# Kernel optimization log

Hardware: AMD Instinct MI355X
Metric: run time of the kernel (lower is better)

## Reference

```python
import jax, jax.numpy as jnp
import numpy as np

L, B, E = 128, 16, 512
C_OUT = 64
KERNELS = [1, 3, 5, 7]
M = len(KERNELS) * C_OUT          # mlpdec_in = 256
OUT_SIZE = 256
SLOPE = 0.1


def setup_inputs() -> dict:
    key = jax.random.key(0)
    ks = jax.random.split(key, 32)
    s = 0.02
    d = {"x": jax.random.normal(ks[0], (L, B, E), dtype=jnp.float32)}
    # conv branches: weight (C_out, 1, k, E), bias (C_out,)
    for i, k in enumerate(KERNELS):
        d[f"cw{i}"] = jax.random.normal(ks[1 + 2 * i], (C_OUT, 1, k, E), dtype=jnp.float32) * s
        d[f"cb{i}"] = jnp.zeros((C_OUT,), dtype=jnp.float32)
    dims = [(C_OUT, 2 * M), (C_OUT, C_OUT), (C_OUT, C_OUT), (C_OUT, C_OUT)]
    for i, (o, inn) in enumerate(dims):
        d[f"mw{i}"] = jax.random.normal(ks[10 + 2 * i], (o, inn), dtype=jnp.float32) * s
        d[f"mb{i}"] = jnp.zeros((o,), dtype=jnp.float32)
    # mlp_layer: Linear(C->C), Linear(C->output_size)
    d["lw0"] = jax.random.normal(ks[20], (C_OUT, C_OUT), dtype=jnp.float32) * s
    d["lb0"] = jnp.zeros((C_OUT,), dtype=jnp.float32)
    d["lw1"] = jax.random.normal(ks[21], (OUT_SIZE, C_OUT), dtype=jnp.float32) * s
    d["lb1"] = jnp.zeros((OUT_SIZE,), dtype=jnp.float32)
    return d


def _lrelu(x):
    return jax.nn.leaky_relu(x, SLOPE)


def _conv_branch(xb, w, b):
    # xb: (B,1,L,E), w: (C,1,k,E) -> (B,C,L)
    k = w.shape[2]
    pad = (k - 1) // 2
    y = jax.lax.conv_general_dilated(
        xb, w, window_strides=(1, 1), padding=[(pad, pad), (0, 0)],
        dimension_numbers=("NCHW", "OIHW", "NCHW"))
    return _lrelu(y[..., 0] + b[None, :, None])


def reference(x, cw0, cb0, cw1, cb1, cw2, cb2, cw3, cb3,
              mw0, mb0, mw1, mb1, mw2, mb2, mw3, mb3,
              lw0, lb0, lw1, lb1):
    # x: (L,B,E) -> (B,1,L,E)
    xb = jnp.transpose(x, (1, 0, 2))[:, None, :, :]
    feats = jnp.concatenate([
        _conv_branch(xb, cw0, cb0), _conv_branch(xb, cw1, cb1),
        _conv_branch(xb, cw2, cb2), _conv_branch(xb, cw3, cb3)], axis=1)  # (B, 4C, L)
    f = jnp.transpose(feats, (2, 0, 1))  # (L, B, M)
    # pairwise: pair[i, j] = [f[j], f[i]]  -> (L, L, B, 2M)
    a = jnp.broadcast_to(f[None, :, :, :], (L, L, B, M))
    bpart = jnp.broadcast_to(f[:, None, :, :], (L, L, B, M))
    h = jnp.concatenate([a, bpart], axis=-1)
    for w, bb in ((mw0, mb0), (mw1, mb1), (mw2, mb2), (mw3, mb3)):
        h = _lrelu(h @ w.T + bb)
    h = h.sum(axis=0)  # (L, B, C)
    h = _lrelu(h @ lw0.T + lb0)
    return _lrelu(h @ lw1.T + lb1)  # (L, B, OUT_SIZE)
```

## Files before the change

### kernel.cpp

```cpp
#include <hip/hip_runtime.h>
#include <hip/hip_bf16.h>

#define SLOPE 0.1f
typedef unsigned short u16;
typedef unsigned int u32;
typedef __attribute__((ext_vector_type(8))) short short8;
typedef __attribute__((ext_vector_type(4))) float floatx4;

__device__ __forceinline__ float lrelu(float x) { return x > 0.0f ? x : SLOPE * x; }

__device__ __forceinline__ void split_rn(float x, u16* h, u16* l) {
    union { __hip_bfloat16 b; u16 u; } c1, c2;
    c1.b = __float2bfloat16(x);
    float hf = __bfloat162float(c1.b);
    c2.b = __float2bfloat16(x - hf);
    *h = c1.u; *l = c2.u;
}

__device__ __forceinline__ void pack2x2(float v0, float v1, u32& h, u32& l) {
    u32 a0 = __float_as_uint(v0), a1 = __float_as_uint(v1);
    h = __builtin_amdgcn_perm(a1, a0, 0x07060302u);
    float r0 = v0 - __uint_as_float(a0 & 0xFFFF0000u);
    float r1 = v1 - __uint_as_float(a1 & 0xFFFF0000u);
    l = __builtin_amdgcn_perm(__float_as_uint(r1), __float_as_uint(r0), 0x07060302u);
}

__device__ __forceinline__ short8 load_frag(const u16* p) {
    union { uint4 q; short8 s; } cv;
    cv.q = *(const uint4*)p;
    return cv.s;
}

__device__ __forceinline__ floatx4 mfma16(short8 a, short8 b, floatx4 c) {
    return __builtin_amdgcn_mfma_f32_16x16x32_bf16(a, b, c, 0, 0, 0);
}

__global__ __launch_bounds__(256) void p0_prep(
    const float* __restrict__ x,
    const float* __restrict__ cw0, const float* __restrict__ cw1,
    const float* __restrict__ cw2, const float* __restrict__ cw3,
    const float* __restrict__ mw0, const float* __restrict__ mw1,
    const float* __restrict__ mw2, const float* __restrict__ mw3,
    const float* __restrict__ lw0, const float* __restrict__ lw1,
    u16* __restrict__ xfh, u16* __restrict__ xfl,
    u16* __restrict__ wcfh, u16* __restrict__ wcfl,
    u16* __restrict__ b2fh, u16* __restrict__ b2fl,
    u16* __restrict__ w3fh, u16* __restrict__ w3fl,
    float* __restrict__ lw0t, float* __restrict__ lw1t)
{
    int idx = (blockIdx.x * 256 + threadIdx.x) * 4;
    if (idx < 1048576) {
        const int j = idx & 7, lane = (idx >> 3) & 63;
        const int kc = (idx >> 9) & 15, rt = idx >> 13;
        const int l15 = lane & 15, quad = lane >> 4;
        const float4 s = *(const float4*)(x + (rt * 16 + l15) * 512 + kc * 32 + quad * 8 + j);
        u16 h[4], l[4];
        split_rn(s.x, &h[0], &l[0]); split_rn(s.y, &h[1], &l[1]);
        split_rn(s.z, &h[2], &l[2]); split_rn(s.w, &h[3], &l[3]);
        *(ushort4*)(xfh + idx) = make_ushort4(h[0], h[1], h[2], h[3]);
        *(ushort4*)(xfl + idx) = make_ushort4(l[0], l[1], l[2], l[3]);
        return;
    }
    idx -= 1048576;
    if (idx < 524288) {
        const int j = idx & 7, lane = (idx >> 3) & 63;
        const int kc = (idx >> 9) & 15, nt = (idx >> 13) & 3, slot = idx >> 15;
        int branch, base;
        if (slot == 0)      { branch = 0; base = 0; }
        else if (slot < 4)  { branch = 1; base = 1; }
        else if (slot < 9)  { branch = 2; base = 4; }
        else                { branch = 3; base = 9; }
        const int dk = slot - base, ksz = 2 * branch + 1;
        const float* cw = branch == 0 ? cw0 : branch == 1 ? cw1 : branch == 2 ? cw2 : cw3;
        const int c = nt * 16 + (lane & 15);
        const int e = kc * 32 + (lane >> 4) * 8 + j;
        const float4 s = *(const float4*)(cw + (c * ksz + dk) * 512 + e);
        u16 h[4], l[4];
        split_rn(s.x, &h[0], &l[0]); split_rn(s.y, &h[1], &l[1]);
        split_rn(s.z, &h[2], &l[2]); split_rn(s.w, &h[3], &l[3]);
        *(ushort4*)(wcfh + idx) = make_ushort4(h[0], h[1], h[2], h[3]);
        *(ushort4*)(wcfl + idx) = make_ushort4(l[0], l[1], l[2], l[3]);
        return;
    }
    idx -= 524288;
    if (idx < 32768) {
        const int j = idx & 7, lane = (idx >> 3) & 63;
        const int kc = (idx >> 9) & 7, nt = (idx >> 12) & 3, nh = idx >> 14;
        const int n = nh * 64 + nt * 16 + (lane & 15);
        const int k = kc * 32 + (lane >> 4) * 8 + j;
        const float4 s = *(const float4*)(mw0 + (n & 63) * 512 + (n >> 6) * 256 + k);
        u16 h[4], l[4];
        split_rn(s.x, &h[0], &l[0]); split_rn(s.y, &h[1], &l[1]);
        split_rn(s.z, &h[2], &l[2]); split_rn(s.w, &h[3], &l[3]);
        *(ushort4*)(b2fh + idx) = make_ushort4(h[0], h[1], h[2], h[3]);
        *(ushort4*)(b2fl + idx) = make_ushort4(l[0], l[1], l[2], l[3]);
        return;
    }
    idx -= 32768;
    if (idx < 12288) {
        const int j = idx & 7, lane = (idx >> 3) & 63;
        const int kc = (idx >> 9) & 1, mt = (idx >> 10) & 3, layer = idx >> 12;
        const float* mw = layer == 0 ? mw1 : layer == 1 ? mw2 : mw3;
        const int ch = mt * 16 + (lane & 15);
        const int k = kc * 32 + (lane >> 4) * 8 + j;
        const float4 s = *(const float4*)(mw + ch * 64 + k);
        u16 h[4], l[4];
        split_rn(s.x, &h[0], &l[0]); split_rn(s.y, &h[1], &l[1]);
        split_rn(s.z, &h[2], &l[2]); split_rn(s.w, &h[3], &l[3]);
        *(ushort4*)(w3fh + idx) = make_ushort4(h[0], h[1], h[2], h[3]);
        *(ushort4*)(w3fl + idx) = make_ushort4(l[0], l[1], l[2], l[3]);
        return;
    }
    idx -= 12288;
    if (idx < 4096) {
        const int k = idx >> 6, n = idx & 63;
        float4 o;
        o.x = lw0[(n + 0) * 64 + k]; o.y = lw0[(n + 1) * 64 + k];
        o.z = lw0[(n + 2) * 64 + k]; o.w = lw0[(n + 3) * 64 + k];
        *(float4*)(lw0t + idx) = o;
        return;
    }
    idx -= 4096;
    if (idx < 16384) {
        const int k = idx >> 8, n = idx & 255;
        float4 o;
        o.x = lw1[(n + 0) * 64 + k]; o.y = lw1[(n + 1) * 64 + k];
        o.z = lw1[(n + 2) * 64 + k]; o.w = lw1[(n + 3) * 64 + k];
        *(float4*)(lw1t + idx) = o;
        return;
    }
}

__global__ __launch_bounds__(512) void k1f_conv(
    const u16* __restrict__ xfh, const u16* __restrict__ xfl,
    const u16* __restrict__ wcfh, const u16* __restrict__ wcfl,
    float* __restrict__ Fp)
{
    __shared__ float P[8][16][72];

    const int t = threadIdx.x, lane = t & 63, w = t >> 6;
    const int rtp = blockIdx.x;
    const int slot = blockIdx.y;
    int br, base;
    if (slot == 0)      { br = 0; base = 0; }
    else if (slot < 4)  { br = 1; base = 1; }
    else if (slot < 9)  { br = 2; base = 4; }
    else                { br = 3; base = 9; }
    const int dk = slot - base;
    const int l15 = lane & 15, quad = lane >> 4;

    floatx4 acc[2][4];
    #pragma unroll
    for (int r = 0; r < 2; ++r)
        #pragma unroll
        for (int j = 0; j < 4; ++j) acc[r][j] = (floatx4)0.0f;

    #pragma unroll
    for (int kk = 0; kk < 2; ++kk) {
        const int kc = w * 2 + kk;
        short8 bh[4], bl[4];
        #pragma unroll
        for (int nt = 0; nt < 4; ++nt) {
            const int boff = (((slot * 4 + nt) * 16 + kc) * 64 + lane) * 8;
            bh[nt] = load_frag(wcfh + boff);
            bl[nt] = load_frag(wcfl + boff);
        }
        #pragma unroll
        for (int r = 0; r < 2; ++r) {
            const int rts = rtp + r * 64 + dk - br;
            if (rts < 0 || rts >= 128) continue;
            const int aoff = ((rts * 16 + kc) * 64 + lane) * 8;
            const short8 ah = load_frag(xfh + aoff);
            const short8 al = load_frag(xfl + aoff);
            #pragma unroll
            for (int nt = 0; nt < 4; ++nt) {
                acc[r][nt] = mfma16(ah, bh[nt], acc[r][nt]);
                acc[r][nt] = mfma16(ah, bl[nt], acc[r][nt]);
                acc[r][nt] = mfma16(al, bh[nt], acc[r][nt]);
            }
        }
    }

    #pragma unroll
    for (int r = 0; r < 2; ++r) {
        #pragma unroll
        for (int nt = 0; nt < 4; ++nt)
            #pragma unroll
            for (int rr = 0; rr < 4; ++rr)
                P[w][quad * 4 + rr][nt * 16 + l15] = acc[r][nt][rr];
        __syncthreads();
        if (t < 256) {
            const int row = t >> 4, c4 = (t & 15) * 4;
            float4 o;
            #pragma unroll
            for (int i = 0; i < 4; ++i) {
                float val = P[0][row][c4 + i];
                #pragma unroll
                for (int ww = 1; ww < 8; ++ww) val += P[ww][row][c4 + i];
                (&o.x)[i] = val;
            }
            const int rowg = (rtp + r * 64) * 16 + row;
            *(float4*)(Fp + (slot * 2048 + rowg) * 64 + c4) = o;
        }
        __syncthreads();
    }
}

__global__ __launch_bounds__(256) void kB_uv(
    const float* __restrict__ Fp,
    const u16* __restrict__ b2fh, const u16* __restrict__ b2fl,
    const float* __restrict__ cb0, const float* __restrict__ cb1,
    const float* __restrict__ cb2, const float* __restrict__ cb3,
    const float* __restrict__ mb0,
    float* __restrict__ u, float* __restrict__ v_t)
{
    __shared__ float P[4][16][17];

    const int t = threadIdx.x, lane = t & 63, w = t >> 6;
    const int bid = blockIdx.x;
    const int rt = bid >> 3;
    const int nh = (bid >> 2) & 1;
    const int nt = bid & 3;
    const int l15 = lane & 15, quad = lane >> 4;

    floatx4 acc = (floatx4)0.0f;

    #pragma unroll
    for (int kk = 0; kk < 2; ++kk) {
        const int kc = w * 2 + kk;
        const int br2 = kc >> 1;
        const int base2 = br2 * br2, ksz2 = 2 * br2 + 1;
        const int cc0 = (kc & 1) * 32 + quad * 8;
        const int row = rt * 16 + l15;

        float s[8];
        #pragma unroll
        for (int j = 0; j < 8; ++j) s[j] = 0.0f;
        for (int d = 0; d < ksz2; ++d) {
            const float* pp = Fp + ((base2 + d) * 2048 + row) * 64 + cc0;
            const float4 q0 = *(const float4*)pp;
            const float4 q1 = *(const float4*)(pp + 4);
            s[0] += q0.x; s[1] += q0.y; s[2] += q0.z; s[3] += q0.w;
            s[4] += q1.x; s[5] += q1.y; s[6] += q1.z; s[7] += q1.w;
        }
        const float* cb = br2 == 0 ? cb0 : br2 == 1 ? cb1 : br2 == 2 ? cb2 : cb3;
        union { u16 us[8]; short8 v; } AH, AL;
        #pragma unroll
        for (int j = 0; j < 8; ++j) {
            const float val = lrelu(s[j] + cb[cc0 + j]);
            split_rn(val, &AH.us[j], &AL.us[j]);
        }
        const short8 ah = AH.v, al = AL.v;

        const int boff = (((nh * 4 + nt) * 8 + kc) * 64 + lane) * 8;
        const short8 bh = load_frag(b2fh + boff);
        const short8 bl = load_frag(b2fl + boff);
        acc = mfma16(ah, bh, acc);
        acc = mfma16(ah, bl, acc);
        acc = mfma16(al, bh, acc);
    }

    #pragma unroll
    for (int rr = 0; rr < 4; ++rr)
        P[w][quad * 4 + rr][l15] = acc[rr];
    __syncthreads();

    {
        const int row = t >> 4, c = t & 15;
        const float val = P[0][row][c] + P[1][row][c] + P[2][row][c] + P[3][row][c];
        const int rglob = rt * 16 + row;
        const int ch = nt * 16 + c;
        if (nh == 0) {
            u[rglob * 64 + ch] = val + mb0[ch];
        } else {
            const int i = rglob >> 4, b = rglob & 15;
            v_t[(b * 128 + i) * 64 + ch] = val;
        }
    }
}

__global__ __launch_bounds__(256, 4) void k3_pair(
    const float* __restrict__ u, const float* __restrict__ v_t,
    const u16* __restrict__ w3fh, const u16* __restrict__ w3fl,
    const float* __restrict__ mb1, const float* __restrict__ mb2,
    const float* __restrict__ mb3,
    const float* __restrict__ lw0t, const float* __restrict__ lb0,
    const float* __restrict__ lw1t, const float* __restrict__ lb1,
    float* __restrict__ out)
{
    __shared__ __align__(16) u16 Hh[128][72];
    __shared__ __align__(16) u16 Hl[128][72];
    __shared__ float Sp[4][64];
    __shared__ float Ss[64];
    __shared__ float T1[64];

    const int t = threadIdx.x, lane = t & 63, w = t >> 6;
    const int jb = blockIdx.x, b = jb & 15;
    const int l15 = lane & 15, quad = lane >> 4;
    const int i0 = w * 32;
    const int c4 = l15 * 4;

    const float4 uu = *(const float4*)(u + jb * 64 + c4);

    const float* vb = v_t + (b * 128 + i0) * 64;
    #pragma unroll
    for (int n = 0; n < 8; ++n) {
        const int idx = n * 64 + lane;
        const int il = idx >> 4;
        const float4 vv = *(const float4*)(vb + idx * 4);
        const float a0 = lrelu(vv.x + uu.x), a1 = lrelu(vv.y + uu.y);
        const float a2 = lrelu(vv.z + uu.z), a3 = lrelu(vv.w + uu.w);
        u32 h01, l01, h23, l23;
        pack2x2(a0, a1, h01, l01);
        pack2x2(a2, a3, h23, l23);
        *(uint2*)&Hh[i0 + il][c4] = make_uint2(h01, h23);
        *(uint2*)&Hl[i0 + il][c4] = make_uint2(l01, l23);
    }

    const float* mbp[3] = {mb1, mb2, mb3};
    for (int layer = 0; layer < 3; ++layer) {
        floatx4 acc[4][2];
        #pragma unroll
        for (int i = 0; i < 4; ++i)
            #pragma unroll
            for (int j = 0; j < 2; ++j) acc[i][j] = (floatx4)0.0f;

        #pragma unroll
        for (int kc = 0; kc < 2; ++kc) {
            short8 ah[4], al[4];
            #pragma unroll
            for (int mt = 0; mt < 4; ++mt) {
                const int aoff = (((layer * 4 + mt) * 2 + kc) * 64 + lane) * 8;
                ah[mt] = load_frag(w3fh + aoff);
                al[mt] = load_frag(w3fl + aoff);
            }
            const int k0 = kc * 32 + quad * 8;
            #pragma unroll
            for (int nt = 0; nt < 2; ++nt) {
                const short8 bh = load_frag(&Hh[i0 + nt * 16 + l15][k0]);
                const short8 bl = load_frag(&Hl[i0 + nt * 16 + l15][k0]);
                #pragma unroll
                for (int mt = 0; mt < 4; ++mt) {
                    acc[mt][nt] = mfma16(ah[mt], bh, acc[mt][nt]);
                    acc[mt][nt] = mfma16(ah[mt], bl, acc[mt][nt]);
                    acc[mt][nt] = mfma16(al[mt], bh, acc[mt][nt]);
                }
            }
        }

        if (layer < 2) {
            #pragma unroll
            for (int mt = 0; mt < 4; ++mt) {
                float bias[4];
                #pragma unroll
                for (int r = 0; r < 4; ++r) bias[r] = mbp[layer][mt * 16 + quad * 4 + r];
                #pragma unroll
                for (int nt = 0; nt < 2; ++nt) {
                    const int i = i0 + nt * 16 + l15;
                    const float v0 = lrelu(acc[mt][nt][0] + bias[0]);
                    const float v1 = lrelu(acc[mt][nt][1] + bias[1]);
                    const float v2 = lrelu(acc[mt][nt][2] + bias[2]);
                    const float v3 = lrelu(acc[mt][nt][3] + bias[3]);
                    u32 h01, l01, h23, l23;
                    pack2x2(v0, v1, h01, l01);
                    pack2x2(v2, v3, h23, l23);
                    *(uint2*)&Hh[i][mt * 16 + quad * 4] = make_uint2(h01, h23);
                    *(uint2*)&Hl[i][mt * 16 + quad * 4] = make_uint2(l01, l23);
                }
            }
        } else {
            #pragma unroll
            for (int mt = 0; mt < 4; ++mt) {
                float bias[4];
                #pragma unroll
                for (int r = 0; r < 4; ++r) bias[r] = mbp[2][mt * 16 + quad * 4 + r];
                float4 sv;
                #pragma unroll
                for (int r = 0; r < 4; ++r) {
                    float val = lrelu(acc[mt][0][r] + bias[r])
                              + lrelu(acc[mt][1][r] + bias[r]);
                    val += __shfl_xor(val, 1, 16);
                    val += __shfl_xor(val, 2, 16);
                    val += __shfl_xor(val, 4, 16);
                    val += __shfl_xor(val, 8, 16);
                    (&sv.x)[r] = val;
                }
                if (l15 == 0)
                    *(float4*)(&Sp[w][mt * 16 + quad * 4]) = sv;
            }
        }
    }

    __syncthreads();
    if (t < 64) Ss[t] = Sp[0][t] + Sp[1][t] + Sp[2][t] + Sp[3][t];
    __syncthreads();
    if (t < 64) {
        float a = lb0[t];
        #pragma unroll 8
        for (int k = 0; k < 64; ++k) a += Ss[k] * lw0t[k * 64 + t];
        T1[t] = lrelu(a);
    }
    __syncthreads();
    {
        float a = lb1[t];
        #pragma unroll 8
        for (int k = 0; k < 64; ++k) a += T1[k] * lw1t[k * 256 + t];
        out[jb * 256 + t] = lrelu(a);
    }
}

extern "C" void kernel_launch(void* const* d_in, const int* in_sizes, int n_in,
                              void* d_out, int out_size, void* d_ws, size_t ws_size,
                              hipStream_t stream)
{
    const float* x   = (const float*)d_in[0];
    const float* cw0 = (const float*)d_in[1];
    const float* cb0 = (const float*)d_in[2];
    const float* cw1 = (const float*)d_in[3];
    const float* cb1 = (const float*)d_in[4];
    const float* cw2 = (const float*)d_in[5];
    const float* cb2 = (const float*)d_in[6];
    const float* cw3 = (const float*)d_in[7];
    const float* cb3 = (const float*)d_in[8];
    const float* mw0 = (const float*)d_in[9];
    const float* mb0 = (const float*)d_in[10];
    const float* mw1 = (const float*)d_in[11];
    const float* mb1 = (const float*)d_in[12];
    const float* mw2 = (const float*)d_in[13];
    const float* mb2 = (const float*)d_in[14];
    const float* mw3 = (const float*)d_in[15];
    const float* mb3 = (const float*)d_in[16];
    const float* lw0 = (const float*)d_in[17];
    const float* lb0 = (const float*)d_in[18];
    const float* lw1 = (const float*)d_in[19];
    const float* lb1 = (const float*)d_in[20];
    float* out = (float*)d_out;

    char* base = (char*)d_ws;
    u16* xfh   = (u16*)(base + 0);
    u16* xfl   = (u16*)(base + 2097152);
    u16* wcfh  = (u16*)(base + 4194304);
    u16* wcfl  = (u16*)(base + 5242880);
    u16* b2fh  = (u16*)(base + 6291456);
    u16* b2fl  = (u16*)(base + 6356992);
    u16* w3fh  = (u16*)(base + 6422528);
    u16* w3fl  = (u16*)(base + 6447104);
    float* lw0t  = (float*)(base + 6471680);
    float* lw1t  = (float*)(base + 6488064);
    float* Fp  = (float*)(base + 6553600);
    float* u   = (float*)(base + 14942208);
    float* v_t = (float*)(base + 15466496);

    hipLaunchKernelGGL(p0_prep, dim3(1600), dim3(256), 0, stream,
                       x, cw0, cw1, cw2, cw3, mw0, mw1, mw2, mw3, lw0, lw1,
                       xfh, xfl, wcfh, wcfl, b2fh, b2fl, w3fh, w3fl, lw0t, lw1t);
    hipLaunchKernelGGL(k1f_conv, dim3(64, 16), dim3(512), 0, stream,
                       xfh, xfl, wcfh, wcfl, Fp);
    hipLaunchKernelGGL(kB_uv, dim3(1024), dim3(256), 0, stream,
                       Fp, b2fh, b2fl, cb0, cb1, cb2, cb3, mb0, u, v_t);
    hipLaunchKernelGGL(k3_pair, dim3(2048), dim3(256), 0, stream,
                       u, v_t, w3fh, w3fl, mb1, mb2, mb3, lw0t, lb0, lw1t, lb1, out);
}
```

Measured before the change: 153.9 us.

## Pair two output rows per block, split i range, and combine via atomics

Each k3 block now processes two (j,b) output rows over half of the i range. This reuses every loaded weight fragment for twice as many MFMAs and halves the per-block i span. The two blocks that share a pair atomically accumulate their partial sums into a global buffer, and the block that arrives last (found with a counter) runs the final MLP layers. The global buffer and counters are zeroed inside kB_uv, reusing workspace that held xfh and is no longer needed by then. In exchange this adds global atomics, a threadfence, and a last-block handoff, and the float summation order is no longer deterministic.

After: 189.1 us. 1.23x slower.

```diff
diff --git a/kernel.cpp b/kernel.cpp
--- a/kernel.cpp
+++ b/kernel.cpp
@@ -212,12 +212,20 @@
     const float* __restrict__ cb0, const float* __restrict__ cb1,
     const float* __restrict__ cb2, const float* __restrict__ cb3,
     const float* __restrict__ mb0,
-    float* __restrict__ u, float* __restrict__ v_t)
+    float* __restrict__ u, float* __restrict__ v_t,
+    float* __restrict__ Sg, int* __restrict__ cnt)
 {
     __shared__ float P[4][16][17];
 
     const int t = threadIdx.x, lane = t & 63, w = t >> 6;
     const int bid = blockIdx.x;
+
+    {
+        const int gid = bid * 256 + t;
+        if (gid < 131072) Sg[gid] = 0.0f;
+        else if (gid < 132096) cnt[gid - 131072] = 0;
+    }
+
     const int rt = bid >> 3;
     const int nh = (bid >> 2) & 1;
     const int nt = bid & 3;
@@ -279,72 +287,91 @@
     }
 }
 
-__global__ __launch_bounds__(256, 4) void k3_pair(
+__global__ __launch_bounds__(256, 4) void k3_dual(
     const float* __restrict__ u, const float* __restrict__ v_t,
     const u16* __restrict__ w3fh, const u16* __restrict__ w3fl,
     const float* __restrict__ mb1, const float* __restrict__ mb2,
     const float* __restrict__ mb3,
     const float* __restrict__ lw0t, const float* __restrict__ lb0,
     const float* __restrict__ lw1t, const float* __restrict__ lb1,
+    float* __restrict__ Sg, int* __restrict__ cnt,
     float* __restrict__ out)
 {
-    __shared__ __align__(16) u16 Hh[128][72];
-    __shared__ __align__(16) u16 Hl[128][72];
-    __shared__ float Sp[4][64];
-    __shared__ float Ss[64];
-    __shared__ float T1[64];
+    __shared__ __align__(16) char smem[38912];
+    u16 (*Hh0)[72] = (u16(*)[72])(smem);
+    u16 (*Hl0)[72] = (u16(*)[72])(smem + 9216);
+    u16 (*Hh1)[72] = (u16(*)[72])(smem + 18432);
+    u16 (*Hl1)[72] = (u16(*)[72])(smem + 27648);
+    float (*Sp0)[64] = (float(*)[64])(smem + 36864);
+    float (*Sp1)[64] = (float(*)[64])(smem + 37888);
+    float *Ss0 = (float*)(smem + 36864);
+    float *T10 = (float*)(smem + 36864 + 256);
+    float *Ss1 = (float*)(smem + 37888);
+    float *T11 = (float*)(smem + 37888 + 256);
+    int   *flagp = (int*)(smem + 36864 + 512);
 
     const int t = threadIdx.x, lane = t & 63, w = t >> 6;
-    const int jb = blockIdx.x, b = jb & 15;
+    const int bid = blockIdx.x;
+    const int p = bid >> 1, half = bid & 1;
+    const int jb0 = p, jb1 = p + 1024, b = p & 15;
     const int l15 = lane & 15, quad = lane >> 4;
-    const int i0 = w * 32;
+    const int i0l = w * 16;
+    const int il15 = i0l + l15;
     const int c4 = l15 * 4;
 
-    const float4 uu = *(const float4*)(u + jb * 64 + c4);
-
-    const float* vb = v_t + (b * 128 + i0) * 64;
+    const float4 uu0 = *(const float4*)(u + jb0 * 64 + c4);
+    const float4 uu1 = *(const float4*)(u + jb1 * 64 + c4);
+
+    const float* vb = v_t + (b * 128 + half * 64 + i0l) * 64;
     #pragma unroll
-    for (int n = 0; n < 8; ++n) {
+    for (int n = 0; n < 4; ++n) {
         const int idx = n * 64 + lane;
         const int il = idx >> 4;
         const float4 vv = *(const float4*)(vb + idx * 4);
-        const float a0 = lrelu(vv.x + uu.x), a1 = lrelu(vv.y + uu.y);
-        const float a2 = lrelu(vv.z + uu.z), a3 = lrelu(vv.w + uu.w);
-        u32 h01, l01, h23, l23;
-        pack2x2(a0, a1, h01, l01);
-        pack2x2(a2, a3, h23, l23);
-        *(uint2*)&Hh[i0 + il][c4] = make_uint2(h01, h23);
-        *(uint2*)&Hl[i0 + il][c4] = make_uint2(l01, l23);
+        {
+            const float a0 = lrelu(vv.x + uu0.x), a1 = lrelu(vv.y + uu0.y);
+            const float a2 = lrelu(vv.z + uu0.z), a3 = lrelu(vv.w + uu0.w);
+            u32 h01, l01, h23, l23;
+            pack2x2(a0, a1, h01, l01);
+            pack2x2(a2, a3, h23, l23);
+            *(uint2*)&Hh0[i0l + il][c4] = make_uint2(h01, h23);
+            *(uint2*)&Hl0[i0l + il][c4] = make_uint2(l01, l23);
+        }
+        {
+            const float a0 = lrelu(vv.x + uu1.x), a1 = lrelu(vv.y + uu1.y);
+            const float a2 = lrelu(vv.z + uu1.z), a3 = lrelu(vv.w + uu1.w);
+            u32 h01, l01, h23, l23;
+            pack2x2(a0, a1, h01, l01);
+            pack2x2(a2, a3, h23, l23);
+            *(uint2*)&Hh1[i0l + il][c4] = make_uint2(h01, h23);
+            *(uint2*)&Hl1[i0l + il][c4] = make_uint2(l01, l23);
+        }
     }
 
     const float* mbp[3] = {mb1, mb2, mb3};
     for (int layer = 0; layer < 3; ++layer) {
-        floatx4 acc[4][2];
-        #pragma unroll
-        for (int i = 0; i < 4; ++i)
-            #pragma unroll
-            for (int j = 0; j < 2; ++j) acc[i][j] = (floatx4)0.0f;
+        floatx4 acc0[4], acc1[4];
+        #pragma unroll
+        for (int i = 0; i < 4; ++i) { acc0[i] = (floatx4)0.0f; acc1[i] = (floatx4)0.0f; }
 
         #pragma unroll
         for (int kc = 0; kc < 2; ++kc) {
-            short8 ah[4], al[4];
+            const int k0 = kc * 32 + quad * 8;
+            const short8 bh0 = load_frag(&Hh0[il15][k0]);
+            const short8 bl0 = load_frag(&Hl0[il15][k0]);
+            const short8 bh1 = load_frag(&Hh1[il15][k0]);
+            const short8 bl1 = load_frag(&Hl1[il15][k0]);
             #pragma unroll
             for (int mt = 0; mt < 4; ++mt) {
                 const int aoff = (((layer * 4 + mt) * 2 + kc) * 64 + lane) * 8;
-                ah[mt] = load_frag(w3fh + aoff);
-                al[mt] = load_frag(w3fl + aoff);
-            }
-            const int k0 = kc * 32 + quad * 8;
-            #pragma unroll
-            for (int nt = 0; nt < 2; ++nt) {
-                const short8 bh = load_frag(&Hh[i0 + nt * 16 + l15][k0]);
-                const short8 bl = load_frag(&Hl[i0 + nt * 16 + l15][k0]);
-                #pragma unroll
-                for (int mt = 0; mt < 4; ++mt) {
-                    acc[mt][nt] = mfma16(ah[mt], bh, acc[mt][nt]);
-                    acc[mt][nt] = mfma16(ah[mt], bl, acc[mt][nt]);
-                    acc[mt][nt] = mfma16(al[mt], bh, acc[mt][nt]);
-                }
+                const short8 ah = load_frag(w3fh + aoff);
+                const short8 al = load_frag(w3fl + aoff);
+                acc0[mt] = mfma16(ah, bh0, acc0[mt]);
+                acc0[mt] = mfma16(ah, bl0, acc0[mt]);
+                acc0[mt] = mfma16(al, bh0, acc0[mt]);
+                acc1[mt] = mfma16(ah, bh1, acc1[mt]);
+                acc1[mt] = mfma16(ah, bl1, acc1[mt]);
+                acc1[mt] = mfma16(al, bh1, acc1[mt]);
             }
         }
 
@@ -354,18 +381,27 @@
                 float bias[4];
                 #pragma unroll
                 for (int r = 0; r < 4; ++r) bias[r] = mbp[layer][mt * 16 + quad * 4 + r];
-                #pragma unroll
-                for (int nt = 0; nt < 2; ++nt) {
-                    const int i = i0 + nt * 16 + l15;
-                    const float v0 = lrelu(acc[mt][nt][0] + bias[0]);
-                    const float v1 = lrelu(acc[mt][nt][1] + bias[1]);
-                    const float v2 = lrelu(acc[mt][nt][2] + bias[2]);
-                    const float v3 = lrelu(acc[mt][nt][3] + bias[3]);
+                {
+                    const float v0 = lrelu(acc0[mt][0] + bias[0]);
+                    const float v1 = lrelu(acc0[mt][1] + bias[1]);
+                    const float v2 = lrelu(acc0[mt][2] + bias[2]);
+                    const float v3 = lrelu(acc0[mt][3] + bias[3]);
                     u32 h01, l01, h23, l23;
                     pack2x2(v0, v1, h01, l01);
                     pack2x2(v2, v3, h23, l23);
-                    *(uint2*)&Hh[i][mt * 16 + quad * 4] = make_uint2(h01, h23);
-                    *(uint2*)&Hl[i][mt * 16 + quad * 4] = make_uint2(l01, l23);
+                    *(uint2*)&Hh0[il15][mt * 16 + quad * 4] = make_uint2(h01, h23);
+                    *(uint2*)&Hl0[il15][mt * 16 + quad * 4] = make_uint2(l01, l23);
+                }
+                {
+                    const float v0 = lrelu(acc1[mt][0] + bias[0]);
+                    const float v1 = lrelu(acc1[mt][1] + bias[1]);
+                    const float v2 = lrelu(acc1[mt][2] + bias[2]);
+                    const float v3 = lrelu(acc1[mt][3] + bias[3]);
+                    u32 h01, l01, h23, l23;
+                    pack2x2(v0, v1, h01, l01);
+                    pack2x2(v2, v3, h23, l23);
+                    *(uint2*)&Hh1[il15][mt * 16 + quad * 4] = make_uint2(h01, h23);
+                    *(uint2*)&Hl1[il15][mt * 16 + quad * 4] = make_uint2(l01, l23);
                 }
             }
         } else {
@@ -374,38 +410,71 @@
                 float bias[4];
                 #pragma unroll
                 for (int r = 0; r < 4; ++r) bias[r] = mbp[2][mt * 16 + quad * 4 + r];
-                float4 sv;
+                float4 sv0, sv1;
                 #pragma unroll
                 for (int r = 0; r < 4; ++r) {
-                    float val = lrelu(acc[mt][0][r] + bias[r])
-                              + lrelu(acc[mt][1][r] + bias[r]);
-                    val += __shfl_xor(val, 1, 16);
-                    val += __shfl_xor(val, 2, 16);
-                    val += __shfl_xor(val, 4, 16);
-                    val += __shfl_xor(val, 8, 16);
-                    (&sv.x)[r] = val;
+                    float v0 = lrelu(acc0[mt][r] + bias[r]);
+                    v0 += __shfl_xor(v0, 1, 16);
+                    v0 += __shfl_xor(v0, 2, 16);
+                    v0 += __shfl_xor(v0, 4, 16);
+                    v0 += __shfl_xor(v0, 8, 16);
+                    (&sv0.x)[r] = v0;
+                    float v1 = lrelu(acc1[mt][r] + bias[r]);
+                    v1 += __shfl_xor(v1, 1, 16);
+                    v1 += __shfl_xor(v1, 2, 16);
+                    v1 += __shfl_xor(v1, 4, 16);
+                    v1 += __shfl_xor(v1, 8, 16);
+                    (&sv1.x)[r] = v1;
                 }
-                if (l15 == 0)
-                    *(float4*)(&Sp[w][mt * 16 + quad * 4]) = sv;
+                if (l15 == 0) {
+                    *(float4*)(&Sp0[w][mt * 16 + quad * 4]) = sv0;
+                    *(float4*)(&Sp1[w][mt * 16 + quad * 4]) = sv1;
+                }
             }
         }
     }
 
     __syncthreads();
-    if (t < 64) Ss[t] = Sp[0][t] + Sp[1][t] + Sp[2][t] + Sp[3][t];
+    if (t < 64) {
+        const float s0 = Sp0[0][t] + Sp0[1][t] + Sp0[2][t] + Sp0[3][t];
+        const float s1 = Sp1[0][t] + Sp1[1][t] + Sp1[2][t] + Sp1[3][t];
+        atomicAdd(Sg + jb0 * 64 + t, s0);
+        atomicAdd(Sg + jb1 * 64 + t, s1);
+    }
+    __syncthreads();
+    if (t == 0) {
+        __threadfence();
+        *flagp = atomicAdd(&cnt[p], 1);
+    }
+    __syncthreads();
+    if (*flagp != 1) return;
+
+    if (t < 64)       Ss0[t] = atomicAdd(&Sg[jb0 * 64 + t], 0.0f);
+    else if (t < 128) Ss1[t - 64] = atomicAdd(&Sg[jb1 * 64 + (t - 64)], 0.0f);
     __syncthreads();
     if (t < 64) {
         float a = lb0[t];
         #pragma unroll 8
-        for (int k = 0; k < 64; ++k) a += Ss[k] * lw0t[k * 64 + t];
-        T1[t] = lrelu(a);
+        for (int k = 0; k < 64; ++k) a += Ss0[k] * lw0t[k * 64 + t];
+        T10[t] = lrelu(a);
+    } else if (t < 128) {
+        const int tt = t - 64;
+        float a = lb0[tt];
+        #pragma unroll 8
+        for (int k = 0; k < 64; ++k) a += Ss1[k] * lw0t[k * 64 + tt];
+        T11[tt] = lrelu(a);
     }
     __syncthreads();
     {
-        float a = lb1[t];
+        float a0 = lb1[t], a1 = lb1[t];
         #pragma unroll 8
-        for (int k = 0; k < 64; ++k) a += T1[k] * lw1t[k * 256 + t];
-        out[jb * 256 + t] = lrelu(a);
+        for (int k = 0; k < 64; ++k) {
+            const float wv = lw1t[k * 256 + t];
+            a0 += T10[k] * wv;
+            a1 += T11[k] * wv;
+        }
+        out[jb0 * 256 + t] = lrelu(a0);
+        out[jb1 * 256 + t] = lrelu(a1);
     }
 }
 
@@ -450,6 +519,8 @@
     float* Fp  = (float*)(base + 6553600);
     float* u   = (float*)(base + 14942208);
     float* v_t = (float*)(base + 15466496);
+    float* Sg  = (float*)(base + 0);
+    int*   cnt = (int*)  (base + 524288);
 
     hipLaunchKernelGGL(p0_prep, dim3(1600), dim3(256), 0, stream,
                        x, cw0, cw1, cw2, cw3, mw0, mw1, mw2, mw3, lw0, lw1,
@@ -457,7 +528,8 @@
     hipLaunchKernelGGL(k1f_conv, dim3(64, 16), dim3(512), 0, stream,
                        xfh, xfl, wcfh, wcfl, Fp);
     hipLaunchKernelGGL(kB_uv, dim3(1024), dim3(256), 0, stream,
-                       Fp, b2fh, b2fl, cb0, cb1, cb2, cb3, mb0, u, v_t);
-    hipLaunchKernelGGL(k3_pair, dim3(2048), dim3(256), 0, stream,
-                       u, v_t, w3fh, w3fl, mb1, mb2, mb3, lw0t, lb0, lw1t, lb1, out);
-}
+                       Fp, b2fh, b2fl, cb0, cb1, cb2, cb3, mb0, u, v_t, Sg, cnt);
+    hipLaunchKernelGGL(k3_dual, dim3(2048), dim3(256), 0, stream,
+                       u, v_t, w3fh, w3fl, mb1, mb2, mb3, lw0t, lb0, lw1t, lb1,
+                       Sg, cnt, out);
+}
```
